# Kernel optimization log

Measured on AMD Instinct MI355X. Metric: run time of the kernel, lower is better.

The kernel has to match this reference:

```python
import jax, jax.numpy as jnp
import numpy as np

B, IN_CH, OUT_CH, STYLE_DIM, K, H, W = 16, 512, 512, 512, 3, 32, 32


def setup_inputs() -> dict:
    key = jax.random.key(0)
    k1, k2, k3, k4 = jax.random.split(key, 4)
    return {
        "x": jax.random.normal(k1, (B, IN_CH, H, W), dtype=jnp.float32),
        "style": jax.random.normal(k2, (B, STYLE_DIM), dtype=jnp.float32),
        "aff_weight": jax.random.normal(k3, (IN_CH, STYLE_DIM), dtype=jnp.float32),
        "aff_bias": jnp.zeros((IN_CH,), dtype=jnp.float32),
        "conv_weight": jax.random.normal(k4, (OUT_CH, IN_CH, K, K), dtype=jnp.float32),
    }


def reference(x, style, aff_weight, aff_bias, conv_weight):
    # EqualizedLinearAct with act='linear': y = style @ (W*scale)^T + bias
    style_dim = aff_weight.shape[1]
    aff_scale = 1.0 / np.sqrt(style_dim)  # gain=1.0
    s = style @ (aff_weight * aff_scale).T + aff_bias + 1.0  # [B, in]

    out_ch, in_ch, k, _ = conv_weight.shape
    w_scale = 1.0 / np.sqrt(in_ch * k * k)  # gain / sqrt(in*k*k)
    # per-sample modulated weights: [B, out, in, k, k]
    w = conv_weight[None, :, :, :, :] * s[:, None, :, None, None] * w_scale
    # demodulation
    d = jax.lax.rsqrt(jnp.sum(w * w, axis=(2, 3, 4), keepdims=True) + 1e-8)
    w = w * d

    # groups=B grouped conv == per-sample conv; up=1, flip_weight=True ->
    # plain cross-correlation (same as torch F.conv2d / lax conv default).
    def conv1(xi, wi):
        # xi: [in, H, W], wi: [out, in, k, k]
        return jax.lax.conv_general_dilated(
            xi[None], wi, window_strides=(1, 1), padding="SAME",
            dimension_numbers=("NCHW", "OIHW", "NCHW"))[0]

    return jax.vmap(conv1)(x, w)  # [B, out, H, W]
```

## Files before the change

kernel.cpp:

```cpp
#include <hip/hip_runtime.h>


#define BATCH   16
#define CIN     512
#define COUT    512
#define IMG     32
#define PAD_IMG 34

static constexpr float AFF_SCALE = 0.044194173824159216f;
static constexpr float W_SCALE   = 0.014731391274719739f;

typedef __bf16 bf16x8 __attribute__((ext_vector_type(8)));
typedef float  f32x4  __attribute__((ext_vector_type(4)));

__device__ inline unsigned short f2bf(float f) {
    union { float f; unsigned int u; } v; v.f = f;
    unsigned int u = v.u;
    unsigned int r = (u + 0x7FFFu + ((u >> 16) & 1u)) >> 16;
    return (unsigned short)r;
}

__device__ inline float waveReduceSum(float v) {
    #pragma unroll
    for (int off = 32; off > 0; off >>= 1) v += __shfl_xor(v, off, 64);
    return v;
}

__global__ void prep1(const float* __restrict__ cw,
                      const float* __restrict__ style,
                      const float* __restrict__ aw,
                      const float* __restrict__ ab,
                      unsigned short* __restrict__ w_t,
                      float* __restrict__ wsq,
                      float* __restrict__ s_out) {
    const int tid = threadIdx.x;
    if (blockIdx.x < 1024) {
        __shared__ float wl[2304];
        const float* src = cw + (size_t)blockIdx.x * 2304;
        for (int j = tid; j < 2304; j += 256) wl[j] = src[j];
        __syncthreads();
        const int idx = blockIdx.x * 256 + tid;
        const int base = tid * 9;
        float acc = 0.f;
        #pragma unroll
        for (int e = 0; e < 9; ++e) {
            float v = wl[base + e];
            acc += v * v;
            w_t[e * (COUT * CIN) + idx] = f2bf(v);
        }
        wsq[idx] = acc;
    } else {
        const int q = blockIdx.x - 1024;
        const int b = q >> 7;
        const int i = (q & 127) * 4 + (tid >> 6);
        const int lane = tid & 63;
        float sum = 0.f;
        #pragma unroll
        for (int k = 0; k < 512; k += 64)
            sum += style[b * 512 + k + lane] * aw[i * 512 + k + lane];
        sum = waveReduceSum(sum);
        if (lane == 0)
            s_out[b * 512 + i] = sum * AFF_SCALE + ab[i] + 1.0f;
    }
}

__global__ void prep2(const float* __restrict__ x,
                      const float* __restrict__ s_in,
                      const float* __restrict__ wsq,
                      unsigned short* __restrict__ xpad,
                      float* __restrict__ scl) {
    const int tid = threadIdx.x;
    if (blockIdx.x >= 4352) {
        const int q = blockIdx.x - 4352;
        const int b = q >> 7;
        const int o = (q & 127) * 4 + (tid >> 6);
        const int lane = tid & 63;
        float sum = 0.f;
        #pragma unroll
        for (int i = 0; i < 512; i += 64) {
            float sv = s_in[b * 512 + i + lane];
            sum += sv * sv * wsq[o * 512 + i + lane];
        }
        sum = waveReduceSum(sum);
        if (lane == 0)
            scl[b * 512 + o] = W_SCALE * rsqrtf(W_SCALE * W_SCALE * sum + 1e-8f);
        return;
    }
    const int c0   = blockIdx.x & 7;
    const int rest = blockIdx.x >> 3;
    const int hh   = rest % 34;
    const int b    = rest / 34;
    const int c0b  = c0 * 64;
    unsigned short* rowbase = xpad + (((size_t)b * PAD_IMG + hh) * PAD_IMG) * 512;

    if (hh == 0 || hh == PAD_IMG - 1) {
        for (int j = tid; j < 34 * 32; j += 256) {
            int ww = j >> 5, cp = (j & 31) * 2;
            *(unsigned int*)(rowbase + (size_t)ww * 512 + c0b + cp) = 0u;
        }
        return;
    }

    __shared__ float t[64][33];
    const int h = hh - 1;
    {
        const int wx = tid & 31;
        const int cb = (tid >> 5) * 8;
        const float* xb = x + (((size_t)b * 512 + c0b + cb) * IMG + h) * IMG + wx;
        #pragma unroll
        for (int j = 0; j < 8; ++j)
            t[cb + j][wx] = xb[(size_t)j * (IMG * IMG)] * s_in[b * 512 + c0b + cb + j];
    }
    __syncthreads();
    {
        const int p  = tid >> 3;
        const int cc = (tid & 7) * 8;
        unsigned short* dst = rowbase + (size_t)(p + 1) * 512 + c0b + cc;
        uint4 pk;
        pk.x = (unsigned)f2bf(t[cc + 0][p]) | ((unsigned)f2bf(t[cc + 1][p]) << 16);
        pk.y = (unsigned)f2bf(t[cc + 2][p]) | ((unsigned)f2bf(t[cc + 3][p]) << 16);
        pk.z = (unsigned)f2bf(t[cc + 4][p]) | ((unsigned)f2bf(t[cc + 5][p]) << 16);
        pk.w = (unsigned)f2bf(t[cc + 6][p]) | ((unsigned)f2bf(t[cc + 7][p]) << 16);
        *(uint4*)dst = pk;
    }
    if (tid < 64) {
        int ww = (tid >> 5) ? (PAD_IMG - 1) : 0;
        int cp = (tid & 31) * 2;
        *(unsigned int*)(rowbase + (size_t)ww * 512 + c0b + cp) = 0u;
    }
}


#define LOADSTEP(stp) do {                                                    \
    const int e_  = (stp) >> 3;                                               \
    const int kc_ = ((stp) & 7) << 6;                                         \
    const int kh_ = (e_ * 11) >> 5;                                           \
    const int kw_ = e_ - kh_ * 3;                                             \
    const unsigned short* Ab_ = wt + (size_t)e_ * (COUT * CIN)                \
                                   + (size_t)m0 * 512 + kc_;                  \
    const unsigned short* Bb_ = xpad + bImgBase                               \
                              + (size_t)((h0 + kh_) * PAD_IMG + kw_) * 512    \
                              + kc_;                                          \
    ra0 = *(const uint4*)(Ab_ + aOff0);                                       \
    ra1 = *(const uint4*)(Ab_ + aOff1);                                       \
    ra2 = *(const uint4*)(Ab_ + aOff2);                                       \
    ra3 = *(const uint4*)(Ab_ + aOff3);                                       \
    rb0 = *(const uint4*)(Bb_ + bOff0);                                       \
    rb1 = *(const uint4*)(Bb_ + bOff1);                                       \
    rb2 = *(const uint4*)(Bb_ + bOff2);                                       \
    rb3 = *(const uint4*)(Bb_ + bOff3);                                       \
} while (0)

__global__ __launch_bounds__(256, 2) void conv_mfma(
    const unsigned short* __restrict__ wt,
    const unsigned short* __restrict__ xpad,
    const float* __restrict__ scl,
    float* __restrict__ out)
{
    __shared__ __align__(16) unsigned short Alds[2][128 * 64];
    __shared__ __align__(16) unsigned short Blds[2][128 * 64];
    __shared__ float sclds[128];

    const int tid = threadIdx.x;
    const int id    = blockIdx.x;
    const int xcd   = id & 7;
    const int local = id >> 3;
    const int gp    = xcd * 16 + (local >> 2);
    const int m0  = (local & 3) * 128;
    const int h0  = (gp & 7) * 4;
    const int b   = gp >> 3;

    if (tid < 128) sclds[tid] = scl[b * 512 + m0 + tid];

    const int wid  = tid >> 6;
    const int lane = tid & 63;
    const int wm = wid & 1, wn = wid >> 1;

    const f32x4 vzero = {0.f, 0.f, 0.f, 0.f};
    f32x4 acc[4][4];
    #pragma unroll
    for (int i = 0; i < 4; ++i)
        #pragma unroll
        for (int j = 0; j < 4; ++j) acc[i][j] = vzero;

    int aOff0, aOff1, aOff2, aOff3;
    int bOff0, bOff1, bOff2, bOff3;
    int lOff0, lOff1, lOff2, lOff3;
    {
        int f, row, c, p;
        f = tid;             row = f >> 3; c = f & 7; p = c ^ (row & 7);
        aOff0 = row * 512 + c * 8;
        bOff0 = ((row >> 5) * PAD_IMG + (row & 31)) * 512 + c * 8;
        lOff0 = row * 64 + p * 8;
        f = 256 + tid;       row = f >> 3; c = f & 7; p = c ^ (row & 7);
        aOff1 = row * 512 + c * 8;
        bOff1 = ((row >> 5) * PAD_IMG + (row & 31)) * 512 + c * 8;
        lOff1 = row * 64 + p * 8;
        f = 512 + tid;       row = f >> 3; c = f & 7; p = c ^ (row & 7);
        aOff2 = row * 512 + c * 8;
        bOff2 = ((row >> 5) * PAD_IMG + (row & 31)) * 512 + c * 8;
        lOff2 = row * 64 + p * 8;
        f = 768 + tid;       row = f >> 3; c = f & 7; p = c ^ (row & 7);
        aOff3 = row * 512 + c * 8;
        bOff3 = ((row >> 5) * PAD_IMG + (row & 31)) * 512 + c * 8;
        lOff3 = row * 64 + p * 8;
    }

    const size_t bImgBase = (size_t)b * PAD_IMG * PAD_IMG * 512;

    uint4 ra0, ra1, ra2, ra3, rb0, rb1, rb2, rb3;

    LOADSTEP(0);

    const int rl   = lane & 15;
    const int kch  = lane >> 4;
    const int sw   = rl & 7;
    const int swz0 = (kch ^ sw) * 8;
    const int swz1 = ((kch + 4) ^ sw) * 8;
    const int arow = (wm * 64 + rl) * 64;
    const int brow = (wn * 64 + rl) * 64;

    for (int step = 0; step < 72; ++step) {
        const int buf = step & 1;
        *(uint4*)(&Alds[buf][lOff0]) = ra0;
        *(uint4*)(&Alds[buf][lOff1]) = ra1;
        *(uint4*)(&Alds[buf][lOff2]) = ra2;
        *(uint4*)(&Alds[buf][lOff3]) = ra3;
        *(uint4*)(&Blds[buf][lOff0]) = rb0;
        *(uint4*)(&Blds[buf][lOff1]) = rb1;
        *(uint4*)(&Blds[buf][lOff2]) = rb2;
        *(uint4*)(&Blds[buf][lOff3]) = rb3;
        const int nxt = step + 1 < 72 ? step + 1 : 71;
        LOADSTEP(nxt);
        __syncthreads();

        {
            bf16x8 af[4], bfr[4];
            #pragma unroll
            for (int mi = 0; mi < 4; ++mi)
                af[mi] = *(const bf16x8*)(&Alds[buf][arow + mi * (16 * 64) + swz0]);
            #pragma unroll
            for (int ni = 0; ni < 4; ++ni)
                bfr[ni] = *(const bf16x8*)(&Blds[buf][brow + ni * (16 * 64) + swz0]);
            #pragma unroll
            for (int mi = 0; mi < 4; ++mi)
                #pragma unroll
                for (int ni = 0; ni < 4; ++ni)
                    acc[mi][ni] = __builtin_amdgcn_mfma_f32_16x16x32_bf16(
                        af[mi], bfr[ni], acc[mi][ni], 0, 0, 0);
        }
        {
            bf16x8 af[4], bfr[4];
            #pragma unroll
            for (int mi = 0; mi < 4; ++mi)
                af[mi] = *(const bf16x8*)(&Alds[buf][arow + mi * (16 * 64) + swz1]);
            #pragma unroll
            for (int ni = 0; ni < 4; ++ni)
                bfr[ni] = *(const bf16x8*)(&Blds[buf][brow + ni * (16 * 64) + swz1]);
            #pragma unroll
            for (int mi = 0; mi < 4; ++mi)
                #pragma unroll
                for (int ni = 0; ni < 4; ++ni)
                    acc[mi][ni] = __builtin_amdgcn_mfma_f32_16x16x32_bf16(
                        af[mi], bfr[ni], acc[mi][ni], 0, 0, 0);
        }
    }

    const int colp = lane & 15;
    const int rowq = (lane >> 4) * 4;
    const int p0 = h0 * 32;
    #pragma unroll
    for (int mi = 0; mi < 4; ++mi) {
        #pragma unroll
        for (int ni = 0; ni < 4; ++ni) {
            const int p = p0 + wn * 64 + ni * 16 + colp;
            #pragma unroll
            for (int r2 = 0; r2 < 4; ++r2) {
                const int ol = wm * 64 + mi * 16 + rowq + r2;
                out[(((size_t)b * 512 + m0 + ol) << 10) + p] =
                    acc[mi][ni][r2] * sclds[ol];
            }
        }
    }
}

extern "C" void kernel_launch(void* const* d_in, const int* in_sizes, int n_in,
                              void* d_out, int out_size, void* d_ws, size_t ws_size,
                              hipStream_t stream) {
    const float* x     = (const float*)d_in[0];
    const float* style = (const float*)d_in[1];
    const float* aw    = (const float*)d_in[2];
    const float* ab    = (const float*)d_in[3];
    const float* cw    = (const float*)d_in[4];
    float* out = (float*)d_out;

    char* ws = (char*)d_ws;
    float* s_buf          = (float*)(ws);
    float* scl            = (float*)(ws + 32768);
    float* wsq            = (float*)(ws + 65536);
    unsigned short* w_t   = (unsigned short*)(ws + 1114112);
    unsigned short* x_pad = (unsigned short*)(ws + 5832704);

    prep1<<<dim3(3072), 256, 0, stream>>>(cw, style, aw, ab, w_t, wsq, s_buf);
    prep2<<<dim3(6400), 256, 0, stream>>>(x, s_buf, wsq, x_pad, scl);
    conv_mfma<<<dim3(512), 256, 0, stream>>>(w_t, x_pad, scl, out);
}
```

Measured before the change: 178.1 us.

## Load activation fragments directly from global into registers, bypassing LDS

The B operand (padded input image) is no longer staged through shared memory. Each lane loads its MFMA fragment straight from global memory at the start of each step. This removes the B LDS buffers, their stores and their reads, cuts shared-memory use and is meant to raise occupancy. In exchange, each wave issues its own uncoalesced-ish global loads, duplicated across the two M-waves, and the loads are no longer prefetched a step ahead, so their latency may be exposed. The MFMAs are also wrapped in s_setprio.

Result: slower. 244.3 us (+37.2%).

```diff
diff --git a/kernel.cpp b/kernel.cpp
--- a/kernel.cpp
+++ b/kernel.cpp
@@ -131,24 +131,32 @@
 }
 
 
-#define LOADSTEP(stp) do {                                                    \
+#define LOADA(stp) do {                                                       \
+    const int e_  = (stp) >> 3;                                               \
+    const int kc_ = ((stp) & 7) << 6;                                         \
+    const unsigned short* Ab_ = wt + (size_t)e_ * (COUT * CIN)                \
+                                   + (size_t)m0 * 512 + kc_;                  \
+    ra0 = *(const uint4*)(Ab_ + aOff0);                                       \
+    ra1 = *(const uint4*)(Ab_ + aOff1);                                       \
+    ra2 = *(const uint4*)(Ab_ + aOff2);                                       \
+    ra3 = *(const uint4*)(Ab_ + aOff3);                                       \
+} while (0)
+
+#define LOADB(stp) do {                                                       \
     const int e_  = (stp) >> 3;                                               \
     const int kc_ = ((stp) & 7) << 6;                                         \
     const int kh_ = (e_ * 11) >> 5;                                           \
     const int kw_ = e_ - kh_ * 3;                                             \
-    const unsigned short* Ab_ = wt + (size_t)e_ * (COUT * CIN)                \
-                                   + (size_t)m0 * 512 + kc_;                  \
     const unsigned short* Bb_ = xpad + bImgBase                               \
-                              + (size_t)((h0 + kh_) * PAD_IMG + kw_) * 512    \
-                              + kc_;                                          \
-    ra0 = *(const uint4*)(Ab_ + aOff0);                                       \
-    ra1 = *(const uint4*)(Ab_ + aOff1);                                       \
-    ra2 = *(const uint4*)(Ab_ + aOff2);                                       \
-    ra3 = *(const uint4*)(Ab_ + aOff3);                                       \
-    rb0 = *(const uint4*)(Bb_ + bOff0);                                       \
-    rb1 = *(const uint4*)(Bb_ + bOff1);                                       \
-    rb2 = *(const uint4*)(Bb_ + bOff2);                                       \
-    rb3 = *(const uint4*)(Bb_ + bOff3);                                       \
+        + (size_t)((h0 + kh_) * PAD_IMG + kw_) * 512 + kc_;                   \
+    pb0 = *(const uint4*)(Bb_ + pOff0);                                       \
+    pb1 = *(const uint4*)(Bb_ + pOff1);                                       \
+    pb2 = *(const uint4*)(Bb_ + pOff2);                                       \
+    pb3 = *(const uint4*)(Bb_ + pOff3);                                       \
+    pb4 = *(const uint4*)(Bb_ + pOff0 + 32);                                  \
+    pb5 = *(const uint4*)(Bb_ + pOff1 + 32);                                  \
+    pb6 = *(const uint4*)(Bb_ + pOff2 + 32);                                  \
+    pb7 = *(const uint4*)(Bb_ + pOff3 + 32);                                  \
 } while (0)
 
 __global__ __launch_bounds__(256, 2) void conv_mfma(
@@ -158,7 +166,6 @@
     float* __restrict__ out)
 {
     __shared__ __align__(16) unsigned short Alds[2][128 * 64];
-    __shared__ __align__(16) unsigned short Blds[2][128 * 64];
     __shared__ float sclds[128];
 
     const int tid = threadIdx.x;
@@ -184,33 +191,20 @@
         for (int j = 0; j < 4; ++j) acc[i][j] = vzero;
 
     int aOff0, aOff1, aOff2, aOff3;
-    int bOff0, bOff1, bOff2, bOff3;
     int lOff0, lOff1, lOff2, lOff3;
     {
         int f, row, c, p;
         f = tid;             row = f >> 3; c = f & 7; p = c ^ (row & 7);
-        aOff0 = row * 512 + c * 8;
-        bOff0 = ((row >> 5) * PAD_IMG + (row & 31)) * 512 + c * 8;
-        lOff0 = row * 64 + p * 8;
+        aOff0 = row * 512 + c * 8;  lOff0 = row * 64 + p * 8;
         f = 256 + tid;       row = f >> 3; c = f & 7; p = c ^ (row & 7);
-        aOff1 = row * 512 + c * 8;
-        bOff1 = ((row >> 5) * PAD_IMG + (row & 31)) * 512 + c * 8;
-        lOff1 = row * 64 + p * 8;
+        aOff1 = row * 512 + c * 8;  lOff1 = row * 64 + p * 8;
         f = 512 + tid;       row = f >> 3; c = f & 7; p = c ^ (row & 7);
-        aOff2 = row * 512 + c * 8;
-        bOff2 = ((row >> 5) * PAD_IMG + (row & 31)) * 512 + c * 8;
-        lOff2 = row * 64 + p * 8;
+        aOff2 = row * 512 + c * 8;  lOff2 = row * 64 + p * 8;
         f = 768 + tid;       row = f >> 3; c = f & 7; p = c ^ (row & 7);
-        aOff3 = row * 512 + c * 8;
-        bOff3 = ((row >> 5) * PAD_IMG + (row & 31)) * 512 + c * 8;
-        lOff3 = row * 64 + p * 8;
+        aOff3 = row * 512 + c * 8;  lOff3 = row * 64 + p * 8;
     }
 
     const size_t bImgBase = (size_t)b * PAD_IMG * PAD_IMG * 512;
-
-    uint4 ra0, ra1, ra2, ra3, rb0, rb1, rb2, rb3;
-
-    LOADSTEP(0);
 
     const int rl   = lane & 15;
     const int kch  = lane >> 4;
@@ -218,51 +212,80 @@
     const int swz0 = (kch ^ sw) * 8;
     const int swz1 = ((kch + 4) ^ sw) * 8;
     const int arow = (wm * 64 + rl) * 64;
-    const int brow = (wn * 64 + rl) * 64;
+    int pOff0, pOff1, pOff2, pOff3;
+    {
+        int pr;
+        pr = wn * 64 + 0 * 16 + rl;
+        pOff0 = ((pr >> 5) * PAD_IMG + (pr & 31)) * 512 + kch * 8;
+        pr = wn * 64 + 1 * 16 + rl;
+        pOff1 = ((pr >> 5) * PAD_IMG + (pr & 31)) * 512 + kch * 8;
+        pr = wn * 64 + 2 * 16 + rl;
+        pOff2 = ((pr >> 5) * PAD_IMG + (pr & 31)) * 512 + kch * 8;
+        pr = wn * 64 + 3 * 16 + rl;
+        pOff3 = ((pr >> 5) * PAD_IMG + (pr & 31)) * 512 + kch * 8;
+    }
+
+    uint4 ra0, ra1, ra2, ra3;
+    uint4 pb0, pb1, pb2, pb3, pb4, pb5, pb6, pb7;
+
+    LOADA(0);
 
     for (int step = 0; step < 72; ++step) {
         const int buf = step & 1;
+        LOADB(step);
         *(uint4*)(&Alds[buf][lOff0]) = ra0;
         *(uint4*)(&Alds[buf][lOff1]) = ra1;
         *(uint4*)(&Alds[buf][lOff2]) = ra2;
         *(uint4*)(&Alds[buf][lOff3]) = ra3;
-        *(uint4*)(&Blds[buf][lOff0]) = rb0;
-        *(uint4*)(&Blds[buf][lOff1]) = rb1;
-        *(uint4*)(&Blds[buf][lOff2]) = rb2;
-        *(uint4*)(&Blds[buf][lOff3]) = rb3;
         const int nxt = step + 1 < 72 ? step + 1 : 71;
-        LOADSTEP(nxt);
+        LOADA(nxt);
         __syncthreads();
 
         {
-            bf16x8 af[4], bfr[4];
+            bf16x8 af[4];
             #pragma unroll
             for (int mi = 0; mi < 4; ++mi)
                 af[mi] = *(const bf16x8*)(&Alds[buf][arow + mi * (16 * 64) + swz0]);
-            #pragma unroll
-            for (int ni = 0; ni < 4; ++ni)
-                bfr[ni] = *(const bf16x8*)(&Blds[buf][brow + ni * (16 * 64) + swz0]);
-            #pragma unroll
-            for (int mi = 0; mi < 4; ++mi)
-                #pragma unroll
-                for (int ni = 0; ni < 4; ++ni)
-                    acc[mi][ni] = __builtin_amdgcn_mfma_f32_16x16x32_bf16(
-                        af[mi], bfr[ni], acc[mi][ni], 0, 0, 0);
+            const bf16x8 b0 = __builtin_bit_cast(bf16x8, pb0);
+            const bf16x8 b1 = __builtin_bit_cast(bf16x8, pb1);
+            const bf16x8 b2 = __builtin_bit_cast(bf16x8, pb2);
+            const bf16x8 b3 = __builtin_bit_cast(bf16x8, pb3);
+            __builtin_amdgcn_s_setprio(1);
+            #pragma unroll
+            for (int mi = 0; mi < 4; ++mi) {
+                acc[mi][0] = __builtin_amdgcn_mfma_f32_16x16x32_bf16(
+                    af[mi], b0, acc[mi][0], 0, 0, 0);
+                acc[mi][1] = __builtin_amdgcn_mfma_f32_16x16x32_bf16(
+                    af[mi], b1, acc[mi][1], 0, 0, 0);
+                acc[mi][2] = __builtin_amdgcn_mfma_f32_16x16x32_bf16(
+                    af[mi], b2, acc[mi][2], 0, 0, 0);
+                acc[mi][3] = __builtin_amdgcn_mfma_f32_16x16x32_bf16(
+                    af[mi], b3, acc[mi][3], 0, 0, 0);
+            }
+            __builtin_amdgcn_s_setprio(0);
         }
         {
-            bf16x8 af[4], bfr[4];
+            bf16x8 af[4];
             #pragma unroll
             for (int mi = 0; mi < 4; ++mi)
                 af[mi] = *(const bf16x8*)(&Alds[buf][arow + mi * (16 * 64) + swz1]);
-            #pragma unroll
-            for (int ni = 0; ni < 4; ++ni)
-                bfr[ni] = *(const bf16x8*)(&Blds[buf][brow + ni * (16 * 64) + swz1]);
-            #pragma unroll
-            for (int mi = 0; mi < 4; ++mi)
-                #pragma unroll
-                for (int ni = 0; ni < 4; ++ni)
-                    acc[mi][ni] = __builtin_amdgcn_mfma_f32_16x16x32_bf16(
-                        af[mi], bfr[ni], acc[mi][ni], 0, 0, 0);
+            const bf16x8 b4 = __builtin_bit_cast(bf16x8, pb4);
+            const bf16x8 b5 = __builtin_bit_cast(bf16x8, pb5);
+            const bf16x8 b6 = __builtin_bit_cast(bf16x8, pb6);
+            const bf16x8 b7 = __builtin_bit_cast(bf16x8, pb7);
+            __builtin_amdgcn_s_setprio(1);
+            #pragma unroll
+            for (int mi = 0; mi < 4; ++mi) {
+                acc[mi][0] = __builtin_amdgcn_mfma_f32_16x16x32_bf16(
+                    af[mi], b4, acc[mi][0], 0, 0, 0);
+                acc[mi][1] = __builtin_amdgcn_mfma_f32_16x16x32_bf16(
+                    af[mi], b5, acc[mi][1], 0, 0, 0);
+                acc[mi][2] = __builtin_amdgcn_mfma_f32_16x16x32_bf16(
+                    af[mi], b6, acc[mi][2], 0, 0, 0);
+                acc[mi][3] = __builtin_amdgcn_mfma_f32_16x16x32_bf16(
+                    af[mi], b7, acc[mi][3], 0, 0, 0);
+            }
+            __builtin_amdgcn_s_setprio(0);
         }
     }
 
```
